# Kernel optimization log

Hardware: AMD Instinct MI355X
Metric: run time of the kernel (lower is better)

Reference implementation:

```python
import jax, jax.numpy as jnp
import numpy as np

B, N, C = 2048, 64, 384
H, WS, HIDDEN, TEMB = 12, 8, 64, 384
D = C // H


def _rpb_index(ws):
    coords = np.stack(np.meshgrid(np.arange(ws), np.arange(ws), indexing='ij'))  # (2, ws, ws)
    flat = coords.reshape(2, -1)                       # (2, ws*ws)
    rel = flat[:, :, None] - flat[:, None, :]          # (2, N, N)
    rel = rel.transpose(1, 2, 0).copy()                # (N, N, 2)
    rel[..., 0] += ws - 1
    rel[..., 1] += ws - 1
    rel[..., 0] *= 2 * ws - 1
    return rel.sum(-1)                                  # (N, N) int


def setup_inputs() -> dict:
    key = jax.random.key(0)
    ks = jax.random.split(key, 16)
    s = 0.02
    inp = {
        'x': jax.random.normal(ks[0], (B, N, C), jnp.float32),
        'temb': jax.random.normal(ks[1], (B, TEMB), jnp.float32),
        'sigma': jax.random.uniform(ks[2], (B,), jnp.float32, 1e-3, 1.0),
        'qkv_w': jax.random.normal(ks[3], (C, 3 * C), jnp.float32) * s,
        'qkv_b': jax.random.normal(ks[4], (3 * C,), jnp.float32) * s,
        'qkvt_w': jax.random.normal(ks[5], (TEMB, 3 * C), jnp.float32) * s,
        'trunk_w1': jax.random.normal(ks[6], (1, HIDDEN), jnp.float32) * s,
        'trunk_b1': jax.random.normal(ks[7], (HIDDEN,), jnp.float32) * s,
        'trunk_w2': jax.random.normal(ks[8], (HIDDEN, HIDDEN), jnp.float32) * s,
        'trunk_b2': jax.random.normal(ks[9], (HIDDEN,), jnp.float32) * s,
        'gate_w': jax.random.normal(ks[10], (HIDDEN, 1), jnp.float32) * s,
        'gate_b': jnp.zeros((1,), jnp.float32),
        'bias_w': jax.random.normal(ks[11], (HIDDEN, H), jnp.float32) * s,
        'bias_b': jax.random.normal(ks[12], (H,), jnp.float32) * s,
        'proj_w': jax.random.normal(ks[13], (C, C), jnp.float32) * s,
        'proj_b': jax.random.normal(ks[14], (C,), jnp.float32) * s,
        'rpb_table': jax.random.normal(ks[15], ((2 * WS - 1) * (2 * WS - 1), H), jnp.float32) * s,
        'rpb_index': jnp.asarray(_rpb_index(WS), jnp.int32),
    }
    return inp


def reference(x, temb, sigma, qkv_w, qkv_b, qkvt_w, trunk_w1, trunk_b1,
              trunk_w2, trunk_b2, gate_w, gate_b, bias_w, bias_b,
              proj_w, proj_b, rpb_table, rpb_index):
    b, n, c = x.shape
    h, d = H, c // H
    scale = d ** -0.5
    # QKV with time-embedding modulation
    qkv = x @ qkv_w + qkv_b + (temb @ qkvt_w)[:, None, :]        # (B, N, 3C)
    qkv = qkv.reshape(b, n, 3, h, d).transpose(2, 0, 3, 1, 4)     # (3, B, H, N, D)
    q, k, v = qkv[0], qkv[1], qkv[2]
    attn = jnp.einsum('bhnd,bhmd->bhnm', q * scale, k)            # (B, H, N, N)
    # relative position bias
    rpb = rpb_table[rpb_index].transpose(2, 0, 1)                 # (H, N, N)
    attn = attn + rpb[None]
    # noise-conditioned gate and per-head bias
    log_sigma = jnp.log(jnp.clip(sigma, 1e-6))[:, None]           # (B, 1)
    hid = jax.nn.silu(log_sigma @ trunk_w1 + trunk_b1)
    hid = jax.nn.silu(hid @ trunk_w2 + trunk_b2)                  # (B, hidden)
    gate = jax.nn.sigmoid(hid @ gate_w + gate_b).reshape(b, 1, 1, 1)
    nbias = (hid @ bias_w + bias_b).reshape(b, h, 1, 1)
    attn = attn / (1.0 + gate) + nbias
    attn = jax.nn.softmax(attn, axis=-1)
    out = jnp.einsum('bhnm,bhmd->bhnd', attn, v)                  # (B, H, N, D)
    out = out.transpose(0, 2, 1, 3).reshape(b, n, c)
    return out @ proj_w + proj_b
```

## Files before the change

### kernel.cpp

```cpp
#include <hip/hip_runtime.h>

#define B_TOT 2048
#define SEQ 64
#define CH 384
#define NH 12
#define HD 32
#define NC3 1152
#define LDP 392
#define QKS 40
#define VS 72
#define HDSZ 7424
#define QK_SCALE 0.17677669529663687f

typedef __attribute__((ext_vector_type(8))) short short8;
typedef __attribute__((ext_vector_type(4))) short short4v;
typedef __attribute__((ext_vector_type(4))) float f32x4;
typedef unsigned short u16;

__device__ __forceinline__ u16 f2bf(float f) {
  unsigned int u = __float_as_uint(f);
  u += 0x7fffu + ((u >> 16) & 1u);
  return (u16)(u >> 16);
}
__device__ __forceinline__ float bf2f(u16 u) {
  return __uint_as_float(((unsigned int)u) << 16);
}

__device__ __forceinline__ int pswz(int row, int col) {
  return row * 64 + ((((col >> 3) ^ (row & 7)) << 3) | (col & 7));
}

__global__ void k_prep(const float* __restrict__ qkv_w, const float* __restrict__ proj_w,
                       const float* __restrict__ rpb_table, const int* __restrict__ rpb_index,
                       u16* __restrict__ qkvwt, u16* __restrict__ projwt, u16* __restrict__ rpbz)
{
  int idx = blockIdx.x * 256 + threadIdx.x;
  if (idx < CH * NC3) {
    int k = idx / NC3, n = idx - k * NC3;
    qkvwt[n * LDP + k] = f2bf(qkv_w[idx]);
    return;
  }
  idx -= CH * NC3;
  if (idx < CH * CH) {
    int k = idx / CH, n = idx - k * CH;
    projwt[n * LDP + k] = f2bf(proj_w[idx]);
    return;
  }
  idx -= CH * CH;
  if (idx < NH * SEQ * SEQ) {
    int h = idx >> 12, j = (idx >> 6) & 63, q = idx & 63;
    int jt = j >> 4, g4j = (j >> 2) & 3, r = j & 3;
    int qt = q >> 4, q16 = q & 15;
    int dst = (h * 16 + jt * 4 + qt) * 256 + g4j * 64 + q16 * 4 + r;
    rpbz[dst] = f2bf(rpb_table[rpb_index[q * 64 + j] * NH + h]);
  }
}

__global__ void k_trunk(const float* __restrict__ sigma, const float* __restrict__ w1,
                        const float* __restrict__ b1, const float* __restrict__ w2,
                        const float* __restrict__ b2, const float* __restrict__ gw,
                        const float* __restrict__ gb, const float* __restrict__ bw,
                        const float* __restrict__ bb,
                        float* __restrict__ inv1pg, float* __restrict__ nbias)
{
  int b = blockIdx.x, j = threadIdx.x;
  __shared__ float sh[64];
  float ls = logf(fmaxf(sigma[b], 1e-6f));
  float z = fmaf(ls, w1[j], b1[j]);
  z = z / (1.f + __expf(-z));
  sh[j] = z;
  __syncthreads();
  float a = b2[j];
  #pragma unroll 8
  for (int i = 0; i < 64; ++i) a = fmaf(sh[i], w2[i * 64 + j], a);
  a = a / (1.f + __expf(-a));
  __syncthreads();
  sh[j] = a;
  __syncthreads();
  if (j == 0) {
    float zg = gb[0];
    #pragma unroll 8
    for (int i = 0; i < 64; ++i) zg = fmaf(sh[i], gw[i], zg);
    float gate = 1.f / (1.f + __expf(-zg));
    inv1pg[b] = 1.f / (1.f + gate);
  }
  if (j < NH) {
    float zb = bb[j];
    #pragma unroll 8
    for (int i = 0; i < 64; ++i) zb = fmaf(sh[i], bw[i * NH + j], zb);
    nbias[b * NH + j] = zb;
  }
}

__global__ __launch_bounds__(256) void k_tvec(const float* __restrict__ temb,
                                              const float* __restrict__ qkvt_w,
                                              const float* __restrict__ qkv_b,
                                              float* __restrict__ tvec)
{
  __shared__ float st[16 * 384];
  int bi = blockIdx.x;
  int brow = bi / 9, cseg = bi - brow * 9;
  int cb = cseg * 128;
  int tid = threadIdx.x;
  for (int idx = tid; idx < 16 * 384; idx += 256) {
    int r = idx / 384, k = idx - r * 384;
    st[idx] = temb[(brow * 16 + r) * 384 + k];
  }
  __syncthreads();
  int cl = tid & 127, half = tid >> 7;
  float acc[8];
  #pragma unroll
  for (int i = 0; i < 8; ++i) acc[i] = 0.f;
  #pragma unroll 4
  for (int k = 0; k < 384; ++k) {
    float w = qkvt_w[k * NC3 + cb + cl];
    #pragma unroll
    for (int i = 0; i < 8; ++i) acc[i] = fmaf(st[(half * 8 + i) * 384 + k], w, acc[i]);
  }
  float qb = qkv_b[cb + cl];
  #pragma unroll
  for (int i = 0; i < 8; ++i)
    tvec[(brow * 16 + half * 8 + i) * NC3 + cb + cl] = acc[i] + qb;
}

template<int NT>
__device__ __forceinline__ void qkv_tiles(const u16* __restrict__ sx, u16* __restrict__ shd,
                                          const u16* __restrict__ qkvwt,
                                          const float* __restrict__ tvb,
                                          int g, int nt0, int q16, int g4)
{
  const f32x4 fz = {0.f, 0.f, 0.f, 0.f};
  float tv[NT][2]; const u16* bp[NT]; int mh6[NT], hj6[NT], hf6[NT];
  #pragma unroll
  for (int i = 0; i < NT; ++i) {
    int nt = nt0 + i;
    int hj = nt / 6, wi = nt - hj * 6;
    int mh = wi >> 1, hf = wi & 1;
    mh6[i] = mh; hj6[i] = hj; hf6[i] = hf;
    int c = mh * CH + (g * 2 + hj) * HD + hf * 16 + q16;
    tv[i][0] = tvb[c];
    tv[i][1] = tvb[NC3 + c];
    bp[i] = qkvwt + c * LDP + g4 * 8;
  }
  f32x4 acc[8][NT];
  #pragma unroll
  for (int m = 0; m < 8; ++m)
    #pragma unroll
    for (int i = 0; i < NT; ++i) acc[m][i] = fz;
  #pragma unroll 2
  for (int kt = 0; kt < 12; ++kt) {
    short8 af[8];
    #pragma unroll
    for (int m = 0; m < 8; ++m)
      af[m] = *reinterpret_cast<const short8*>(&sx[(m * 16 + q16) * LDP + kt * 32 + g4 * 8]);
    #pragma unroll
    for (int i = 0; i < NT; ++i) {
      short8 bf = *reinterpret_cast<const short8*>(bp[i] + kt * 32);
      #pragma unroll
      for (int m = 0; m < 8; ++m)
        acc[m][i] = __builtin_amdgcn_mfma_f32_16x16x32_bf16(af[m], bf, acc[m][i], 0, 0, 0);
    }
  }
  #pragma unroll
  for (int i = 0; i < NT; ++i) {
    int cof = hf6[i] * 16 + q16;
    #pragma unroll
    for (int m = 0; m < 8; ++m) {
      int bt = m >> 2;
      u16* hbase = &shd[(bt * 2 + hj6[i]) * HDSZ];
      int mrow = (m & 3) * 16 + g4 * 4;
      f32x4 a = acc[m][i];
      float tvv = tv[i][bt];
      if (mh6[i] == 0) {
        #pragma unroll
        for (int r = 0; r < 4; ++r)
          hbase[(mrow + r) * QKS + cof] = f2bf((a[r] + tvv) * QK_SCALE);
      } else if (mh6[i] == 1) {
        #pragma unroll
        for (int r = 0; r < 4; ++r)
          hbase[2560 + (mrow + r) * QKS + cof] = f2bf(a[r] + tvv);
      } else {
        short4v pk;
        #pragma unroll
        for (int r = 0; r < 4; ++r) pk[r] = (short)f2bf(a[r] + tvv);
        *reinterpret_cast<short4v*>(&hbase[5120 + cof * VS + mrow]) = pk;
      }
    }
  }
}

__global__ __launch_bounds__(512, 2) void k_attn(
    const float* __restrict__ x, const float* __restrict__ tvec,
    const float* __restrict__ inv1pg, const float* __restrict__ nbias,
    const u16* __restrict__ qkvwt, const u16* __restrict__ rpbz,
    u16* __restrict__ attw)
{
  __shared__ __align__(16) u16 s_x[128 * LDP];
  __shared__ __align__(16) u16 s_hd[4 * HDSZ];
  const f32x4 fz = {0.f, 0.f, 0.f, 0.f};

  const int b0 = blockIdx.x * 2;
  const int tid = threadIdx.x;
  const int w = tid >> 6, l = tid & 63;
  const int q16 = l & 15, g4 = l >> 4;

  {
    const float* xb = x + (size_t)b0 * (SEQ * CH);
    #pragma unroll 4
    for (int it = 0; it < 24; ++it) {
      int fi = it * 512 + tid;
      int row = fi / 96, c4 = fi - row * 96;
      const float4 a = *reinterpret_cast<const float4*>(xb + fi * 4);
      short4v v;
      v[0] = (short)f2bf(a.x); v[1] = (short)f2bf(a.y);
      v[2] = (short)f2bf(a.z); v[3] = (short)f2bf(a.w);
      *reinterpret_cast<short4v*>(&s_x[row * LDP + c4 * 4]) = v;
    }
  }
  __syncthreads();

  const float invb0 = inv1pg[b0], invb1 = inv1pg[b0 + 1];
  const float* tvb = tvec + (size_t)b0 * NC3;

  const int nt0 = (w < 4) ? 2 * w : 8 + (w - 4);

  for (int g = 0; g < 6; ++g) {
    if (w < 4) qkv_tiles<2>(s_x, s_hd, qkvwt, tvb, g, nt0, q16, g4);
    else       qkv_tiles<1>(s_x, s_hd, qkvwt, tvb, g, nt0, q16, g4);
    __syncthreads();

    f32x4 st2[2][4];
    #pragma unroll
    for (int t = 0; t < 2; ++t) {
      const int tau = w * 2 + t;
      const int cmb = tau >> 2, qt = tau & 3;
      const int bt = cmb >> 1, hh = cmb & 1;
      const int h = g * 2 + hh;
      const u16* sq = &s_hd[cmb * HDSZ];
      const u16* sk = sq + 2560;
      const float inv = bt ? invb1 : invb0;
      const float nb = nbias[(b0 + bt) * NH + h];

      short4v rp4[4];
      #pragma unroll
      for (int jt = 0; jt < 4; ++jt)
        rp4[jt] = *reinterpret_cast<const short4v*>(
            &rpbz[(h * 16 + jt * 4 + qt) * 256 + g4 * 64 + q16 * 4]);

      short8 bq = *reinterpret_cast<const short8*>(&sq[(qt * 16 + q16) * QKS + g4 * 8]);
      #pragma unroll
      for (int jt = 0; jt < 4; ++jt) {
        short8 ak = *reinterpret_cast<const short8*>(&sk[(jt * 16 + q16) * QKS + g4 * 8]);
        st2[t][jt] = __builtin_amdgcn_mfma_f32_16x16x32_bf16(ak, bq, fz, 0, 0, 0);
      }
      float mx = -1e30f;
      #pragma unroll
      for (int jt = 0; jt < 4; ++jt)
        #pragma unroll
        for (int r = 0; r < 4; ++r) {
          float s = fmaf(st2[t][jt][r], inv, fmaf(bf2f((u16)rp4[jt][r]), inv, nb));
          st2[t][jt][r] = s;
          mx = fmaxf(mx, s);
        }
      mx = fmaxf(mx, __shfl_xor(mx, 16));
      mx = fmaxf(mx, __shfl_xor(mx, 32));
      float sum = 0.f;
      #pragma unroll
      for (int jt = 0; jt < 4; ++jt)
        #pragma unroll
        for (int r = 0; r < 4; ++r) {
          float p = __expf(st2[t][jt][r] - mx);
          st2[t][jt][r] = p;
          sum += p;
        }
      sum += __shfl_xor(sum, 16);
      sum += __shfl_xor(sum, 32);
      float rn = 1.f / sum;
      #pragma unroll
      for (int jt = 0; jt < 4; ++jt)
        #pragma unroll
        for (int r = 0; r < 4; ++r) st2[t][jt][r] *= rn;
    }
    __syncthreads();
    #pragma unroll
    for (int t = 0; t < 2; ++t) {
      const int tau = w * 2 + t;
      const int cmb = tau >> 2, qt = tau & 3;
      const int bt = cmb >> 1, hh = cmb & 1;
      const int h = g * 2 + hh;
      u16* sq = &s_hd[cmb * HDSZ];
      const u16* svt = sq + 5120;
      u16* P = sq;

      #pragma unroll
      for (int jt = 0; jt < 4; ++jt) {
        short4v pk;
        #pragma unroll
        for (int r = 0; r < 4; ++r) pk[r] = (short)f2bf(st2[t][jt][r]);
        *reinterpret_cast<short4v*>(&P[pswz(qt * 16 + q16, jt * 16 + 4 * g4)]) = pk;
      }
      f32x4 o[2];
      o[0] = fz; o[1] = fz;
      #pragma unroll
      for (int kk = 0; kk < 2; ++kk) {
        short8 ap = *reinterpret_cast<const short8*>(
            &P[pswz(qt * 16 + q16, kk * 32 + g4 * 8)]);
        #pragma unroll
        for (int dt = 0; dt < 2; ++dt) {
          short8 bv = *reinterpret_cast<const short8*>(
              &svt[(dt * 16 + q16) * VS + kk * 32 + g4 * 8]);
          o[dt] = __builtin_amdgcn_mfma_f32_16x16x32_bf16(ap, bv, o[dt], 0, 0, 0);
        }
      }
      u16* ab = attw + (size_t)(b0 + bt) * (SEQ * CH);
      #pragma unroll
      for (int dt = 0; dt < 2; ++dt)
        #pragma unroll
        for (int r = 0; r < 4; ++r)
          ab[(qt * 16 + g4 * 4 + r) * CH + h * HD + dt * 16 + q16] = f2bf(o[dt][r]);
    }
    __syncthreads();
  }
}

__global__ __launch_bounds__(512, 2) void k_proj(
    const u16* __restrict__ attw, const u16* __restrict__ projwt,
    const float* __restrict__ proj_b, float* __restrict__ out)
{
  __shared__ __align__(16) u16 s_a[128 * LDP];
  const f32x4 fz = {0.f, 0.f, 0.f, 0.f};
  const int tid = threadIdx.x;
  const int w = tid >> 6, l = tid & 63;
  const int q16 = l & 15, g4 = l >> 4;
  const size_t row0 = (size_t)blockIdx.x * 128;

  {
    const u16* ab = attw + row0 * CH;
    #pragma unroll 4
    for (int it = 0; it < 12; ++it) {
      int slot = it * 512 + tid;
      int row = slot / 48, c8 = slot - row * 48;
      short8 v = *reinterpret_cast<const short8*>(ab + row * CH + c8 * 8);
      *reinterpret_cast<short8*>(&s_a[row * LDP + c8 * 8]) = v;
    }
  }
  __syncthreads();

  const u16* bpw[3]; float4 pb4[3];
  #pragma unroll
  for (int i = 0; i < 3; ++i) {
    int nt = w * 3 + i;
    bpw[i] = projwt + (nt * 16 + q16) * LDP + g4 * 8;
    pb4[i] = *reinterpret_cast<const float4*>(&proj_b[nt * 16 + 4 * g4]);
  }
  f32x4 acc[8][3];
  #pragma unroll
  for (int m = 0; m < 8; ++m)
    #pragma unroll
    for (int i = 0; i < 3; ++i) acc[m][i] = fz;
  #pragma unroll 2
  for (int kt = 0; kt < 12; ++kt) {
    short8 af[8];
    #pragma unroll
    for (int m = 0; m < 8; ++m)
      af[m] = *reinterpret_cast<const short8*>(&s_a[(m * 16 + q16) * LDP + kt * 32 + g4 * 8]);
    #pragma unroll
    for (int i = 0; i < 3; ++i) {
      short8 bf = *reinterpret_cast<const short8*>(bpw[i] + kt * 32);
      #pragma unroll
      for (int m = 0; m < 8; ++m)
        acc[m][i] = __builtin_amdgcn_mfma_f32_16x16x32_bf16(bf, af[m], acc[m][i], 0, 0, 0);
    }
  }
  float* ob = out + row0 * CH;
  #pragma unroll
  for (int i = 0; i < 3; ++i) {
    int cb = (w * 3 + i) * 16 + 4 * g4;
    #pragma unroll
    for (int m = 0; m < 8; ++m) {
      float4 v;
      v.x = acc[m][i][0] + pb4[i].x;
      v.y = acc[m][i][1] + pb4[i].y;
      v.z = acc[m][i][2] + pb4[i].z;
      v.w = acc[m][i][3] + pb4[i].w;
      *reinterpret_cast<float4*>(&ob[(m * 16 + q16) * CH + cb]) = v;
    }
  }
}

extern "C" void kernel_launch(void* const* d_in, const int* in_sizes, int n_in,
                              void* d_out, int out_size, void* d_ws, size_t ws_size,
                              hipStream_t stream) {
  const float* x       = (const float*)d_in[0];
  const float* temb    = (const float*)d_in[1];
  const float* sigma   = (const float*)d_in[2];
  const float* qkv_w   = (const float*)d_in[3];
  const float* qkv_b   = (const float*)d_in[4];
  const float* qkvt_w  = (const float*)d_in[5];
  const float* w1      = (const float*)d_in[6];
  const float* b1      = (const float*)d_in[7];
  const float* w2      = (const float*)d_in[8];
  const float* b2      = (const float*)d_in[9];
  const float* gw      = (const float*)d_in[10];
  const float* gb      = (const float*)d_in[11];
  const float* bw      = (const float*)d_in[12];
  const float* bb      = (const float*)d_in[13];
  const float* proj_w  = (const float*)d_in[14];
  const float* proj_b  = (const float*)d_in[15];
  const float* rpb_tab = (const float*)d_in[16];
  const int*   rpb_idx = (const int*)d_in[17];
  float* out = (float*)d_out;

  char* ws = (char*)d_ws;
  float* tvec   = (float*)(ws);
  float* inv1pg = (float*)(ws + 9437184);
  float* nbias  = (float*)(ws + 9445376);
  u16*   qkvwt  = (u16*)  (ws + 9543680);
  u16*   projwt = (u16*)  (ws + 10446848);
  u16*   rpbz   = (u16*)  (ws + 10747904);
  u16*   attw   = (u16*)  (ws + 10846208);

  k_prep<<<2496, 256, 0, stream>>>(qkv_w, proj_w, rpb_tab, rpb_idx, qkvwt, projwt, rpbz);
  k_trunk<<<2048, 64, 0, stream>>>(sigma, w1, b1, w2, b2, gw, gb, bw, bb, inv1pg, nbias);
  k_tvec<<<1152, 256, 0, stream>>>(temb, qkvt_w, qkv_b, tvec);
  k_attn<<<1024, 512, 0, stream>>>(x, tvec, inv1pg, nbias, qkvwt, rpbz, attw);
  k_proj<<<1024, 512, 0, stream>>>(attw, projwt, proj_b, out);
}
```

Measured before the change: 436.6 us.

## Merge prep kernels, software-pipeline QKV GEMM in attention, halve proj tile

Folds the three small setup kernels (weight prep, sigma trunk, time-embedding vector) into one launch dispatched by block index, cutting launch overhead. In the attention kernel, the QKV GEMM for the next head group now runs right after softmax and before the PV stage, with the epilogue split out. This lets MFMA work overlap other phases and drops one barrier per group. The projection kernel uses 64-row tiles with twice as many blocks and a higher occupancy hint. The trade-off is that accumulators live across phases, raising register pressure.

```diff
diff --git a/kernel.cpp b/kernel.cpp
--- a/kernel.cpp
+++ b/kernel.cpp
@@ -30,119 +30,118 @@
   return row * 64 + ((((col >> 3) ^ (row & 7)) << 3) | (col & 7));
 }
 
-__global__ void k_prep(const float* __restrict__ qkv_w, const float* __restrict__ proj_w,
-                       const float* __restrict__ rpb_table, const int* __restrict__ rpb_index,
-                       u16* __restrict__ qkvwt, u16* __restrict__ projwt, u16* __restrict__ rpbz)
+__global__ __launch_bounds__(256) void k_aux(
+    const float* __restrict__ qkv_w, const float* __restrict__ proj_w,
+    const float* __restrict__ rpb_table, const int* __restrict__ rpb_index,
+    const float* __restrict__ sigma, const float* __restrict__ w1,
+    const float* __restrict__ b1, const float* __restrict__ w2,
+    const float* __restrict__ b2, const float* __restrict__ gw,
+    const float* __restrict__ gb, const float* __restrict__ bw,
+    const float* __restrict__ bb, const float* __restrict__ temb,
+    const float* __restrict__ qkvt_w, const float* __restrict__ qkv_b,
+    u16* __restrict__ qkvwt, u16* __restrict__ projwt, u16* __restrict__ rpbz,
+    float* __restrict__ inv1pg, float* __restrict__ nbias, float* __restrict__ tvec)
 {
-  int idx = blockIdx.x * 256 + threadIdx.x;
-  if (idx < CH * NC3) {
-    int k = idx / NC3, n = idx - k * NC3;
-    qkvwt[n * LDP + k] = f2bf(qkv_w[idx]);
+  __shared__ float shmem[16 * 384];
+  const int bid = blockIdx.x;
+  const int tid = threadIdx.x;
+
+  if (bid < 2496) {
+    int idx = bid * 256 + tid;
+    if (idx < CH * NC3) {
+      int k = idx / NC3, n = idx - k * NC3;
+      qkvwt[n * LDP + k] = f2bf(qkv_w[idx]);
+      return;
+    }
+    idx -= CH * NC3;
+    if (idx < CH * CH) {
+      int k = idx / CH, n = idx - k * CH;
+      projwt[n * LDP + k] = f2bf(proj_w[idx]);
+      return;
+    }
+    idx -= CH * CH;
+    if (idx < NH * SEQ * SEQ) {
+      int h = idx >> 12, j = (idx >> 6) & 63, q = idx & 63;
+      int jt = j >> 4, g4j = (j >> 2) & 3, r = j & 3;
+      int qt = q >> 4, q16 = q & 15;
+      int dst = (h * 16 + jt * 4 + qt) * 256 + g4j * 64 + q16 * 4 + r;
+      rpbz[dst] = f2bf(rpb_table[rpb_index[q * 64 + j] * NH + h]);
+    }
     return;
   }
-  idx -= CH * NC3;
-  if (idx < CH * CH) {
-    int k = idx / CH, n = idx - k * CH;
-    projwt[n * LDP + k] = f2bf(proj_w[idx]);
+  if (bid < 3008) {
+    float* sh = shmem;
+    const int bt = tid >> 6, j = tid & 63;
+    const int b = (bid - 2496) * 4 + bt;
+    float ls = logf(fmaxf(sigma[b], 1e-6f));
+    float z = fmaf(ls, w1[j], b1[j]);
+    z = z / (1.f + __expf(-z));
+    sh[bt * 64 + j] = z;
+    __syncthreads();
+    float a = b2[j];
+    #pragma unroll 8
+    for (int i = 0; i < 64; ++i) a = fmaf(sh[bt * 64 + i], w2[i * 64 + j], a);
+    a = a / (1.f + __expf(-a));
+    __syncthreads();
+    sh[bt * 64 + j] = a;
+    __syncthreads();
+    if (j == 0) {
+      float zg = gb[0];
+      #pragma unroll 8
+      for (int i = 0; i < 64; ++i) zg = fmaf(sh[bt * 64 + i], gw[i], zg);
+      float gate = 1.f / (1.f + __expf(-zg));
+      inv1pg[b] = 1.f / (1.f + gate);
+    }
+    if (j < NH) {
+      float zb = bb[j];
+      #pragma unroll 8
+      for (int i = 0; i < 64; ++i) zb = fmaf(sh[bt * 64 + i], bw[i * NH + j], zb);
+      nbias[b * NH + j] = zb;
+    }
     return;
   }
-  idx -= CH * CH;
-  if (idx < NH * SEQ * SEQ) {
-    int h = idx >> 12, j = (idx >> 6) & 63, q = idx & 63;
-    int jt = j >> 4, g4j = (j >> 2) & 3, r = j & 3;
-    int qt = q >> 4, q16 = q & 15;
-    int dst = (h * 16 + jt * 4 + qt) * 256 + g4j * 64 + q16 * 4 + r;
-    rpbz[dst] = f2bf(rpb_table[rpb_index[q * 64 + j] * NH + h]);
-  }
-}
-
-__global__ void k_trunk(const float* __restrict__ sigma, const float* __restrict__ w1,
-                        const float* __restrict__ b1, const float* __restrict__ w2,
-                        const float* __restrict__ b2, const float* __restrict__ gw,
-                        const float* __restrict__ gb, const float* __restrict__ bw,
-                        const float* __restrict__ bb,
-                        float* __restrict__ inv1pg, float* __restrict__ nbias)
-{
-  int b = blockIdx.x, j = threadIdx.x;
-  __shared__ float sh[64];
-  float ls = logf(fmaxf(sigma[b], 1e-6f));
-  float z = fmaf(ls, w1[j], b1[j]);
-  z = z / (1.f + __expf(-z));
-  sh[j] = z;
-  __syncthreads();
-  float a = b2[j];
-  #pragma unroll 8
-  for (int i = 0; i < 64; ++i) a = fmaf(sh[i], w2[i * 64 + j], a);
-  a = a / (1.f + __expf(-a));
-  __syncthreads();
-  sh[j] = a;
-  __syncthreads();
-  if (j == 0) {
-    float zg = gb[0];
-    #pragma unroll 8
-    for (int i = 0; i < 64; ++i) zg = fmaf(sh[i], gw[i], zg);
-    float gate = 1.f / (1.f + __expf(-zg));
-    inv1pg[b] = 1.f / (1.f + gate);
-  }
-  if (j < NH) {
-    float zb = bb[j];
-    #pragma unroll 8
-    for (int i = 0; i < 64; ++i) zb = fmaf(sh[i], bw[i * NH + j], zb);
-    nbias[b * NH + j] = zb;
-  }
-}
-
-__global__ __launch_bounds__(256) void k_tvec(const float* __restrict__ temb,
-                                              const float* __restrict__ qkvt_w,
-                                              const float* __restrict__ qkv_b,
-                                              float* __restrict__ tvec)
-{
-  __shared__ float st[16 * 384];
-  int bi = blockIdx.x;
-  int brow = bi / 9, cseg = bi - brow * 9;
-  int cb = cseg * 128;
-  int tid = threadIdx.x;
-  for (int idx = tid; idx < 16 * 384; idx += 256) {
-    int r = idx / 384, k = idx - r * 384;
-    st[idx] = temb[(brow * 16 + r) * 384 + k];
-  }
-  __syncthreads();
-  int cl = tid & 127, half = tid >> 7;
-  float acc[8];
-  #pragma unroll
-  for (int i = 0; i < 8; ++i) acc[i] = 0.f;
-  #pragma unroll 4
-  for (int k = 0; k < 384; ++k) {
-    float w = qkvt_w[k * NC3 + cb + cl];
-    #pragma unroll
-    for (int i = 0; i < 8; ++i) acc[i] = fmaf(st[(half * 8 + i) * 384 + k], w, acc[i]);
-  }
-  float qb = qkv_b[cb + cl];
-  #pragma unroll
-  for (int i = 0; i < 8; ++i)
-    tvec[(brow * 16 + half * 8 + i) * NC3 + cb + cl] = acc[i] + qb;
+  {
+    const int bi = bid - 3008;
+    const int brow = bi / 9, cseg = bi - brow * 9;
+    const int cb = cseg * 128;
+    for (int idx = tid; idx < 16 * 384; idx += 256) {
+      int r = idx / 384, k = idx - r * 384;
+      shmem[idx] = temb[(brow * 16 + r) * 384 + k];
+    }
+    __syncthreads();
+    int cl = tid & 127, half = tid >> 7;
+    float acc[8];
+    #pragma unroll
+    for (int i = 0; i < 8; ++i) acc[i] = 0.f;
+    #pragma unroll 4
+    for (int k = 0; k < 384; ++k) {
+      float w = qkvt_w[k * NC3 + cb + cl];
+      #pragma unroll
+      for (int i = 0; i < 8; ++i) acc[i] = fmaf(shmem[(half * 8 + i) * 384 + k], w, acc[i]);
+    }
+    float qb = qkv_b[cb + cl];
+    #pragma unroll
+    for (int i = 0; i < 8; ++i)
+      tvec[(brow * 16 + half * 8 + i) * NC3 + cb + cl] = acc[i] + qb;
+  }
 }
 
 template<int NT>
-__device__ __forceinline__ void qkv_tiles(const u16* __restrict__ sx, u16* __restrict__ shd,
-                                          const u16* __restrict__ qkvwt,
-                                          const float* __restrict__ tvb,
-                                          int g, int nt0, int q16, int g4)
+__device__ __forceinline__ void gemm_qkv(f32x4 (&acc)[8][2],
+                                         const u16* __restrict__ sx,
+                                         const u16* __restrict__ qkvwt,
+                                         int g, int nt0, int q16, int g4)
 {
   const f32x4 fz = {0.f, 0.f, 0.f, 0.f};
-  float tv[NT][2]; const u16* bp[NT]; int mh6[NT], hj6[NT], hf6[NT];
+  const u16* bp[NT];
   #pragma unroll
   for (int i = 0; i < NT; ++i) {
     int nt = nt0 + i;
     int hj = nt / 6, wi = nt - hj * 6;
     int mh = wi >> 1, hf = wi & 1;
-    mh6[i] = mh; hj6[i] = hj; hf6[i] = hf;
     int c = mh * CH + (g * 2 + hj) * HD + hf * 16 + q16;
-    tv[i][0] = tvb[c];
-    tv[i][1] = tvb[NC3 + c];
     bp[i] = qkvwt + c * LDP + g4 * 8;
   }
-  f32x4 acc[8][NT];
   #pragma unroll
   for (int m = 0; m < 8; ++m)
     #pragma unroll
@@ -161,21 +160,33 @@
         acc[m][i] = __builtin_amdgcn_mfma_f32_16x16x32_bf16(af[m], bf, acc[m][i], 0, 0, 0);
     }
   }
+}
+
+template<int NT>
+__device__ __forceinline__ void epi_qkv(const f32x4 (&acc)[8][2], u16* __restrict__ shd,
+                                        const float* __restrict__ tvb,
+                                        int g, int nt0, int q16, int g4)
+{
   #pragma unroll
   for (int i = 0; i < NT; ++i) {
-    int cof = hf6[i] * 16 + q16;
+    int nt = nt0 + i;
+    int hj = nt / 6, wi = nt - hj * 6;
+    int mh = wi >> 1, hf = wi & 1;
+    int c = mh * CH + (g * 2 + hj) * HD + hf * 16 + q16;
+    float tv0 = tvb[c], tv1 = tvb[NC3 + c];
+    int cof = hf * 16 + q16;
     #pragma unroll
     for (int m = 0; m < 8; ++m) {
       int bt = m >> 2;
-      u16* hbase = &shd[(bt * 2 + hj6[i]) * HDSZ];
+      u16* hbase = &shd[(bt * 2 + hj) * HDSZ];
       int mrow = (m & 3) * 16 + g4 * 4;
       f32x4 a = acc[m][i];
-      float tvv = tv[i][bt];
-      if (mh6[i] == 0) {
+      float tvv = bt ? tv1 : tv0;
+      if (mh == 0) {
         #pragma unroll
         for (int r = 0; r < 4; ++r)
           hbase[(mrow + r) * QKS + cof] = f2bf((a[r] + tvv) * QK_SCALE);
-      } else if (mh6[i] == 1) {
+      } else if (mh == 1) {
         #pragma unroll
         for (int r = 0; r < 4; ++r)
           hbase[2560 + (mrow + r) * QKS + cof] = f2bf(a[r] + tvv);
@@ -224,9 +235,14 @@
 
   const int nt0 = (w < 4) ? 2 * w : 8 + (w - 4);
 
+  f32x4 acc[8][2];
+  if (w < 4) gemm_qkv<2>(acc, s_x, qkvwt, 0, nt0, q16, g4);
+  else       gemm_qkv<1>(acc, s_x, qkvwt, 0, nt0, q16, g4);
+
   for (int g = 0; g < 6; ++g) {
-    if (w < 4) qkv_tiles<2>(s_x, s_hd, qkvwt, tvb, g, nt0, q16, g4);
-    else       qkv_tiles<1>(s_x, s_hd, qkvwt, tvb, g, nt0, q16, g4);
+    if (g) __syncthreads();
+    if (w < 4) epi_qkv<2>(acc, s_hd, tvb, g, nt0, q16, g4);
+    else       epi_qkv<1>(acc, s_hd, tvb, g, nt0, q16, g4);
     __syncthreads();
 
     f32x4 st2[2][4];
@@ -282,6 +298,11 @@
         for (int r = 0; r < 4; ++r) st2[t][jt][r] *= rn;
     }
     __syncthreads();
+
+    if (g < 5) {
+      if (w < 4) gemm_qkv<2>(acc, s_x, qkvwt, g + 1, nt0, q16, g4);
+      else       gemm_qkv<1>(acc, s_x, qkvwt, g + 1, nt0, q16, g4);
+    }
     #pragma unroll
     for (int t = 0; t < 2; ++t) {
       const int tau = w * 2 + t;
@@ -319,25 +340,24 @@
         for (int r = 0; r < 4; ++r)
           ab[(qt * 16 + g4 * 4 + r) * CH + h * HD + dt * 16 + q16] = f2bf(o[dt][r]);
     }
-    __syncthreads();
-  }
-}
-
-__global__ __launch_bounds__(512, 2) void k_proj(
+  }
+}
+
+__global__ __launch_bounds__(512, 4) void k_proj(
     const u16* __restrict__ attw, const u16* __restrict__ projwt,
     const float* __restrict__ proj_b, float* __restrict__ out)
 {
-  __shared__ __align__(16) u16 s_a[128 * LDP];
+  __shared__ __align__(16) u16 s_a[64 * LDP];
   const f32x4 fz = {0.f, 0.f, 0.f, 0.f};
   const int tid = threadIdx.x;
   const int w = tid >> 6, l = tid & 63;
   const int q16 = l & 15, g4 = l >> 4;
-  const size_t row0 = (size_t)blockIdx.x * 128;
+  const size_t row0 = (size_t)blockIdx.x * 64;
 
   {
     const u16* ab = attw + row0 * CH;
-    #pragma unroll 4
-    for (int it = 0; it < 12; ++it) {
+    #pragma unroll
+    for (int it = 0; it < 6; ++it) {
       int slot = it * 512 + tid;
       int row = slot / 48, c8 = slot - row * 48;
       short8 v = *reinterpret_cast<const short8*>(ab + row * CH + c8 * 8);
@@ -353,31 +373,33 @@
     bpw[i] = projwt + (nt * 16 + q16) * LDP + g4 * 8;
     pb4[i] = *reinterpret_cast<const float4*>(&proj_b[nt * 16 + 4 * g4]);
   }
-  f32x4 acc[8][3];
-  #pragma unroll
-  for (int m = 0; m < 8; ++m)
+  f32x4 acc[4][3];
+  #pragma unroll
+  for (int m = 0; m < 4; ++m)
     #pragma unroll
     for (int i = 0; i < 3; ++i) acc[m][i] = fz;
   #pragma unroll 2
   for (int kt = 0; kt < 12; ++kt) {
-    short8 af[8];
-    #pragma unroll
-    for (int m = 0; m < 8; ++m)
+    short8 af[4];
+    #pragma unroll
+    for (int m = 0; m < 4; ++m)
       af[m] = *reinterpret_cast<const short8*>(&s_a[(m * 16 + q16) * LDP + kt * 32 + g4 * 8]);
-    #pragma unroll
-    for (int i = 0; i < 3; ++i) {
-      short8 bf = *reinterpret_cast<const short8*>(bpw[i] + kt * 32);
-      #pragma unroll
-      for (int m = 0; m < 8; ++m)
-        acc[m][i] = __builtin_amdgcn_mfma_f32_16x16x32_bf16(bf, af[m], acc[m][i], 0, 0, 0);
-    }
+    short8 bf[3];
+    #pragma unroll
+    for (int i = 0; i < 3; ++i)
+      bf[i] = *reinterpret_cast<const short8*>(bpw[i] + kt * 32);
+    #pragma unroll
+    for (int i = 0; i < 3; ++i)
+      #pragma unroll
+      for (int m = 0; m < 4; ++m)
+        acc[m][i] = __builtin_amdgcn_mfma_f32_16x16x32_bf16(bf[i], af[m], acc[m][i], 0, 0, 0);
   }
   float* ob = out + row0 * CH;
   #pragma unroll
   for (int i = 0; i < 3; ++i) {
     int cb = (w * 3 + i) * 16 + 4 * g4;
     #pragma unroll
-    for (int m = 0; m < 8; ++m) {
+    for (int m = 0; m < 4; ++m) {
       float4 v;
       v.x = acc[m][i][0] + pb4[i].x;
       v.y = acc[m][i][1] + pb4[i].y;
@@ -420,9 +442,10 @@
   u16*   rpbz   = (u16*)  (ws + 10747904);
   u16*   attw   = (u16*)  (ws + 10846208);
 
-  k_prep<<<2496, 256, 0, stream>>>(qkv_w, proj_w, rpb_tab, rpb_idx, qkvwt, projwt, rpbz);
-  k_trunk<<<2048, 64, 0, stream>>>(sigma, w1, b1, w2, b2, gw, gb, bw, bb, inv1pg, nbias);
-  k_tvec<<<1152, 256, 0, stream>>>(temb, qkvt_w, qkv_b, tvec);
+  k_aux<<<4160, 256, 0, stream>>>(qkv_w, proj_w, rpb_tab, rpb_idx,
+                                  sigma, w1, b1, w2, b2, gw, gb, bw, bb,
+                                  temb, qkvt_w, qkv_b,
+                                  qkvwt, projwt, rpbz, inv1pg, nbias, tvec);
   k_attn<<<1024, 512, 0, stream>>>(x, tvec, inv1pg, nbias, qkvwt, rpbz, attw);
-  k_proj<<<1024, 512, 0, stream>>>(attw, projwt, proj_b, out);
-}
+  k_proj<<<2048, 512, 0, stream>>>(attw, projwt, proj_b, out);
+}
```

New measurement: 411.2 us. 1.06x faster.
